# Kernel optimization log

Hardware: AMD Instinct MI355X
Metric: run time of the kernel (lower is better)

## Reference

```python
import jax, jax.numpy as jnp
import numpy as np

HIDDEN = 2048
HEAD_DIM = 128
Q_HEAD = 16
KV_HEAD = 2
MAX_TOKEN = 4096
THETA = 10000
B = 1
S = 2048
SCALER = 1.0 / np.sqrt(HEAD_DIM)


def make_pos_emb():
    # Faithful port of ROPEEmbedding.create_embedding
    i = np.repeat(np.arange(HEAD_DIM // 2), 2)            # [D]
    freq = np.power(float(THETA), -i * 2.0 / HEAD_DIM)    # [D]
    t = np.einsum('i,j->ij', freq, np.arange(MAX_TOKEN, dtype=np.float64))  # [D, T]
    cos = np.cos(t)
    sin = np.sin(t)
    sin[0::2] *= -1.0                                      # negate even rows (even dim indices)
    pe = np.concatenate([cos, sin], axis=0).T              # [T, 2D]
    return jnp.asarray(pe, jnp.float32)


def _flip_pairs(x):
    # swap adjacent pairs along last dim: (x0,x1,x2,x3,..) -> (x1,x0,x3,x2,..)
    b, h, s, d = x.shape
    return x.reshape(b, h, s, d // 2, 2)[..., ::-1].reshape(b, h, s, d)


def _apply_rope(x, pos_emb):
    # x: [B, H, S, D]; pos_emb: [max_token, 2D]
    s = x.shape[2]
    pe = pos_emb[:s]                     # [S, 2D]
    cos = pe[:, :HEAD_DIM]               # [S, D]
    sin = pe[:, HEAD_DIM:]               # [S, D] (signed)
    return x * cos + _flip_pairs(x) * sin


def setup_inputs() -> dict:
    key = jax.random.key(0)
    ks = jax.random.split(key, 5)
    qkv_out = (Q_HEAD + 2 * KV_HEAD) * HEAD_DIM  # 2560
    lim_qkv = 1.0 / np.sqrt(HIDDEN)
    lim_o = 1.0 / np.sqrt(Q_HEAD * HEAD_DIM)
    x = jax.random.normal(ks[0], (B, S, HIDDEN), dtype=jnp.float32)
    w_qkv = jax.random.uniform(ks[1], (qkv_out, HIDDEN), jnp.float32, -lim_qkv, lim_qkv)
    b_qkv = jax.random.uniform(ks[2], (qkv_out,), jnp.float32, -lim_qkv, lim_qkv)
    w_o = jax.random.uniform(ks[3], (HIDDEN, Q_HEAD * HEAD_DIM), jnp.float32, -lim_o, lim_o)
    b_o = jax.random.uniform(ks[4], (HIDDEN,), jnp.float32, -lim_o, lim_o)
    # causal additive mask, as typically passed to this module
    neg = jnp.float32(-1e9)
    attention_mask = jnp.where(
        jnp.tril(jnp.ones((S, S), dtype=bool)), jnp.float32(0.0), neg
    )[None, None, :, :]
    pos_emb = make_pos_emb()
    return {"tensor": x, "attention_mask": attention_mask, "w_qkv": w_qkv,
            "b_qkv": b_qkv, "w_o": w_o, "b_o": b_o, "pos_emb": pos_emb}


def reference(tensor, attention_mask, w_qkv, b_qkv, w_o, b_o, pos_emb):
    b, s, _ = tensor.shape
    qkv = tensor @ w_qkv.T + b_qkv                        # [B, S, 2560]
    dq = HEAD_DIM * Q_HEAD
    dkv = HEAD_DIM * KV_HEAD
    q = qkv[..., :dq].reshape(b, s, Q_HEAD, HEAD_DIM)
    k = qkv[..., dq:dq + dkv].reshape(b, s, KV_HEAD, HEAD_DIM)
    v = qkv[..., dq + dkv:].reshape(b, s, KV_HEAD, HEAD_DIM)
    scale = Q_HEAD // KV_HEAD
    k = jnp.repeat(k, scale, axis=2)                      # [B, S, Q_HEAD, D]
    v = jnp.repeat(v, scale, axis=2)
    q = q.transpose(0, 2, 1, 3)                           # [B, H, S, D]
    k = k.transpose(0, 2, 1, 3)
    v = v.transpose(0, 2, 1, 3)
    q = _apply_rope(q, pos_emb)
    k = _apply_rope(k, pos_emb)
    scores = jnp.einsum('bhqd,bhkd->bhqk', q, k) * SCALER
    scores = scores + attention_mask
    attn = jax.nn.softmax(scores, axis=-1)
    out = jnp.einsum('bhqk,bhkd->bhqd', attn, v)          # [B, H, S, D]
    out = out.transpose(0, 2, 1, 3).reshape(b, s, Q_HEAD * HEAD_DIM)
    return out @ w_o.T + b_o
```

## Files before the change

### kernel.cpp

```cpp
#include <hip/hip_runtime.h>
#include <stdint.h>

#define SQ 2048
#define DH 128
#define SCALER 0.08838834764831845f

typedef float f32x4 __attribute__((ext_vector_type(4)));
typedef short s16x8 __attribute__((ext_vector_type(8)));
typedef short s16x4 __attribute__((ext_vector_type(4)));

__device__ __forceinline__ short f2bf(float f) {
  uint32_t x = __float_as_uint(f);
  uint32_t r = (x + 0x7fffu + ((x >> 16) & 1u)) >> 16;
  return (short)(r & 0xffffu);
}

__device__ __forceinline__ void mfma16(f32x4& d, s16x8 a, s16x8 b) {
  asm("v_mfma_f32_16x16x32_bf16 %0, %1, %2, %0" : "+v"(d) : "v"(a), "v"(b));
}

__device__ __forceinline__ void gload16(const void* g, void* l) {
  __builtin_amdgcn_global_load_lds(
      (__attribute__((address_space(1))) void*)const_cast<void*>(g),
      (__attribute__((address_space(3))) void*)l, 16, 0, 0);
}

__global__ __launch_bounds__(256) void cvt3_bf16(
    const float* __restrict__ a, const float* __restrict__ b,
    const float* __restrict__ c, short* __restrict__ out,
    int na8, int nb8, int nc8) {
  int i = blockIdx.x * 256 + threadIdx.x;
  if (i >= na8 + nb8 + nc8) return;
  const float* src;
  if (i < na8) src = a + (size_t)i * 8;
  else if (i < na8 + nb8) src = b + (size_t)(i - na8) * 8;
  else src = c + (size_t)(i - na8 - nb8) * 8;
  const float4* p = (const float4*)src;
  float4 u = p[0], v = p[1];
  s16x8 o;
  o[0] = f2bf(u.x); o[1] = f2bf(u.y); o[2] = f2bf(u.z); o[3] = f2bf(u.w);
  o[4] = f2bf(v.x); o[5] = f2bf(v.y); o[6] = f2bf(v.z); o[7] = f2bf(v.w);
  *((s16x8*)out + i) = o;
}

template <int MODE>
__global__ __launch_bounds__(256) void gemm_bt_bias(
    const short* __restrict__ A, const short* __restrict__ B,
    const float* __restrict__ bias, float* __restrict__ C,
    const float* __restrict__ pe, short* __restrict__ qws,
    short* __restrict__ kws, short* __restrict__ vtws,
    int M, int N, int K) {
  __shared__ __align__(16) short As_[2][128 * 64];
  __shared__ __align__(16) short Bs_[2][64 * 64];
  const int t = threadIdx.x;
  const int l = t & 63, w = t >> 6;
  const int wr = w >> 1, wc = w & 1;
  const int lr = l & 15, lk = l >> 4;
  const int m0 = blockIdx.y * 128, n0 = blockIdx.x * 64;

  f32x4 acc[4][2] = {};

#define GSTAGE(buf, kt)                                                         \
  {                                                                             \
    const short* ga = A + (size_t)m0 * K + (kt);                                \
    const short* gb = B + (size_t)n0 * K + (kt);                                \
    _Pragma("unroll") for (int i = 0; i < 4; ++i) {                             \
      int j = i * 256 + t;                                                      \
      int lbase = (i * 256 + (t & ~63)) << 4;                                   \
      gload16(ga + (size_t)(j >> 3) * K + ((j & 7) << 3),                       \
              (char*)As_[buf] + lbase);                                         \
    }                                                                           \
    _Pragma("unroll") for (int i = 0; i < 2; ++i) {                             \
      int j = i * 256 + t;                                                      \
      int lbase = (i * 256 + (t & ~63)) << 4;                                   \
      gload16(gb + (size_t)(j >> 3) * K + ((j & 7) << 3),                       \
              (char*)Bs_[buf] + lbase);                                         \
    }                                                                           \
  }

  GSTAGE(0, 0);
  __syncthreads();

  const int nk = K >> 6;
  for (int ki = 0; ki < nk; ++ki) {
    const int cur = ki & 1;
    if (ki + 1 < nk) GSTAGE(cur ^ 1, (ki + 1) << 6);
    const short* As = As_[cur];
    const short* Bs = Bs_[cur];
#pragma unroll
    for (int ks = 0; ks < 2; ++ks) {
      s16x8 af[4], bg[2];
#pragma unroll
      for (int i = 0; i < 4; ++i)
        af[i] = *(const s16x8*)(As + (wr * 64 + i * 16 + lr) * 64 + ks * 32 + lk * 8);
#pragma unroll
      for (int i = 0; i < 2; ++i)
        bg[i] = *(const s16x8*)(Bs + (wc * 32 + i * 16 + lr) * 64 + ks * 32 + lk * 8);
#pragma unroll
      for (int mi = 0; mi < 4; ++mi)
#pragma unroll
        for (int ni = 0; ni < 2; ++ni)
          mfma16(acc[mi][ni], af[mi], bg[ni]);
    }
    __syncthreads();
  }
#undef GSTAGE

  if (MODE == 0) {
#pragma unroll
    for (int mi = 0; mi < 4; ++mi) {
      int row = m0 + wr * 64 + mi * 16 + lk * 4;
#pragma unroll
      for (int ni = 0; ni < 2; ++ni) {
        int col = n0 + wc * 32 + ni * 16 + lr;
        float bv = bias[col];
#pragma unroll
        for (int r = 0; r < 4; ++r)
          C[(size_t)(row + r) * N + col] = acc[mi][ni][r] + bv;
      }
    }
  } else {
    short* Ct = (short*)As_;
    if (n0 < 2304) {
#pragma unroll
      for (int mi = 0; mi < 4; ++mi) {
        int row_l = wr * 64 + mi * 16 + lk * 4;
#pragma unroll
        for (int ni = 0; ni < 2; ++ni) {
          int col_l = wc * 32 + ni * 16 + lr;
          int col = n0 + col_l;
          float bv = bias[col];
          int d = col & 127;
#pragma unroll
          for (int r = 0; r < 4; ++r) {
            float v = acc[mi][ni][r] + bv;
            float p = __shfl_xor(v, 1);
            int s = m0 + row_l + r;
            const float* per = pe + (size_t)s * 256;
            float y = v * per[d] + p * per[128 + d];
            if (n0 < 2048) y *= SCALER;
            Ct[(row_l + r) * 72 + col_l] = f2bf(y);
          }
        }
      }
      __syncthreads();
      if (n0 < 2048) {
        int hq = n0 >> 7, d0 = n0 & 127;
#pragma unroll
        for (int i = 0; i < 4; ++i) {
          int idx = i * 256 + t;
          int sl = idx >> 3, c = idx & 7;
          s16x8 val = *(const s16x8*)(Ct + sl * 72 + c * 8);
          *(s16x8*)(qws + ((size_t)hq * SQ + m0 + sl) * DH + d0 + c * 8) = val;
        }
      } else {
        int hk = (n0 - 2048) >> 7, d0 = (n0 - 2048) & 127;
#pragma unroll
        for (int i = 0; i < 4; ++i) {
          int idx = i * 256 + t;
          int sl = idx >> 3, c = idx & 7;
          s16x8 val = *(const s16x8*)(Ct + sl * 72 + c * 8);
          int slot = ((d0 >> 3) + c) ^ (sl & 15);
          *(s16x8*)(kws + (size_t)hk * SQ * DH + (size_t)(m0 + sl) * DH + slot * 8) = val;
        }
      }
    } else {
      int hk = (n0 - 2304) >> 7, d0 = (n0 - 2304) & 127;
#pragma unroll
      for (int mi = 0; mi < 4; ++mi) {
        int row_l = wr * 64 + mi * 16 + lk * 4;
#pragma unroll
        for (int ni = 0; ni < 2; ++ni) {
          int col_l = wc * 32 + ni * 16 + lr;
          float bv = bias[n0 + col_l];
#pragma unroll
          for (int r = 0; r < 4; ++r)
            Ct[col_l * 136 + row_l + r] = f2bf(acc[mi][ni][r] + bv);
        }
      }
      __syncthreads();
#pragma unroll
      for (int i = 0; i < 4; ++i) {
        int idx = i * 256 + t;
        int dl = idx >> 4, c = idx & 15;
        s16x8 val = *(const s16x8*)(Ct + dl * 136 + c * 8);
        int d = d0 + dl;
        size_t dst = (size_t)hk * DH * SQ + (size_t)d * SQ +
                     (size_t)((m0 >> 6) + (c >> 3)) * 64 +
                     (size_t)(((c & 7) ^ (d & 7)) << 3);
        *(s16x8*)(vtws + dst) = val;
      }
    }
  }
}

__global__ __launch_bounds__(256) void attn_fwd(
    const short* __restrict__ qws, const short* __restrict__ kws,
    const short* __restrict__ vtws, short* __restrict__ attnws) {
  __shared__ __align__(16) short Ks[2][64 * 128];
  __shared__ __align__(16) short Vt[2][128 * 64];
  __shared__ __align__(16) short Ps[4][16 * 72];

  const int bx = blockIdx.x;
  const int h = bx & 15;
  const int i_ = bx >> 4;
  const int qb = (i_ < 16) ? (31 - i_) : (i_ - 16);
  const int hk = h >> 3;
  const int t = threadIdx.x, l = t & 63, w = t >> 6;
  const int lr = l & 15, lk = l >> 4;

  s16x8 qf[4];
  {
    const short* qbase = qws + ((size_t)h * SQ + (size_t)qb * 64 + w * 16) * DH;
#pragma unroll
    for (int kd = 0; kd < 4; ++kd)
      qf[kd] = *(const s16x8*)(qbase + (size_t)lr * DH + kd * 32 + lk * 8);
  }

  f32x4 o[8] = {};
  float m_ = -1e30f, l_ = 0.f;

  const short* gkh = kws + (size_t)hk * SQ * DH;
  const short* gvh = vtws + (size_t)hk * DH * SQ;

#define STAGE(buf, kb)                                                          \
  {                                                                             \
    const short* gk = gkh + (size_t)(kb)*64 * DH;                               \
    const short* gv = gvh + (size_t)(kb)*64;                                    \
    _Pragma("unroll") for (int i = 0; i < 4; ++i) {                             \
      int j = i * 256 + t;                                                      \
      int lbase = (i * 256 + (t & ~63)) << 4;                                   \
      gload16(gk + (size_t)(j >> 4) * DH + ((j & 15) << 3),                     \
              (char*)Ks[buf] + lbase);                                          \
      gload16(gv + (size_t)(j >> 3) * SQ + ((j & 7) << 3),                      \
              (char*)Vt[buf] + lbase);                                          \
    }                                                                           \
  }

  STAGE(0, 0);
  __syncthreads();

  for (int kb = 0; kb <= qb; ++kb) {
    const int cur = kb & 1;
    if (kb < qb) STAGE(cur ^ 1, kb + 1);

    f32x4 sc_[4] = {};
#pragma unroll
    for (int kd = 0; kd < 4; ++kd) {
#pragma unroll
      for (int nt = 0; nt < 4; ++nt) {
        int krow = nt * 16 + lr;
        int slot = (kd * 4 + lk) ^ lr;
        s16x8 kf = *(const s16x8*)(Ks[cur] + krow * 128 + slot * 8);
        mfma16(sc_[nt], kf, qf[kd]);
      }
    }
    if (kb == qb) {
      int qloc = w * 16 + lr;
#pragma unroll
      for (int nt = 0; nt < 4; ++nt)
#pragma unroll
        for (int r = 0; r < 4; ++r) {
          int col = nt * 16 + lk * 4 + r;
          if (col > qloc) sc_[nt][r] = -1e30f;
        }
    }
    {
      float rm = -1e30f;
#pragma unroll
      for (int nt = 0; nt < 4; ++nt)
        rm = fmaxf(rm, fmaxf(fmaxf(sc_[nt][0], sc_[nt][1]),
                             fmaxf(sc_[nt][2], sc_[nt][3])));
      rm = fmaxf(rm, __shfl_xor(rm, 16));
      rm = fmaxf(rm, __shfl_xor(rm, 32));
      float mn = fmaxf(m_, rm);
      float scl = __expf(m_ - mn);
      float rs = 0.f;
#pragma unroll
      for (int nt = 0; nt < 4; ++nt)
#pragma unroll
        for (int r = 0; r < 4; ++r) {
          sc_[nt][r] = __expf(sc_[nt][r] - mn);
          rs += sc_[nt][r];
        }
      rs += __shfl_xor(rs, 16);
      rs += __shfl_xor(rs, 32);
      l_ = l_ * scl + rs;
      m_ = mn;
#pragma unroll
      for (int dt = 0; dt < 8; ++dt)
#pragma unroll
        for (int r = 0; r < 4; ++r) o[dt][r] *= scl;
    }
    {
      short* ps = (short*)Ps[w];
#pragma unroll
      for (int nt = 0; nt < 4; ++nt)
#pragma unroll
        for (int r = 0; r < 4; ++r)
          ps[lr * 72 + nt * 16 + lk * 4 + r] = f2bf(sc_[nt][r]);
    }
    {
      const short* ps = (const short*)Ps[w];
#pragma unroll
      for (int kp = 0; kp < 2; ++kp) {
        s16x8 pbf = *(const s16x8*)(ps + lr * 72 + kp * 32 + lk * 8);
#pragma unroll
        for (int dt = 0; dt < 8; ++dt) {
          int drow = dt * 16 + lr;
          int slot = (kp * 4 + lk) ^ (lr & 7);
          s16x8 vb = *(const s16x8*)(Vt[cur] + drow * 64 + slot * 8);
          mfma16(o[dt], vb, pbf);
        }
      }
    }
    __syncthreads();
  }
#undef STAGE

  {
    int srow = qb * 64 + w * 16 + lr;
#pragma unroll
    for (int dt = 0; dt < 8; ++dt) {
      s16x4 st;
#pragma unroll
      for (int r = 0; r < 4; ++r) st[r] = f2bf(o[dt][r] / l_);
      *(s16x4*)(attnws + (size_t)srow * 2048 + h * DH + dt * 16 + lk * 4) = st;
    }
  }
}

extern "C" void kernel_launch(void* const* d_in, const int* in_sizes, int n_in,
                              void* d_out, int out_size, void* d_ws, size_t ws_size,
                              hipStream_t stream) {
  (void)in_sizes; (void)n_in; (void)out_size; (void)ws_size;
  const float* x     = (const float*)d_in[0];
  const float* w_qkv = (const float*)d_in[2];
  const float* b_qkv = (const float*)d_in[3];
  const float* w_o   = (const float*)d_in[4];
  const float* b_o   = (const float*)d_in[5];
  const float* pe    = (const float*)d_in[6];
  float* out = (float*)d_out;

  short* xb     = (short*)d_ws;
  short* wqkvb  = xb + (size_t)2048 * 2048;
  short* wob    = wqkvb + (size_t)2560 * 2048;
  short* qws    = wob + (size_t)2048 * 2048;
  short* kws    = qws + (size_t)16 * 2048 * 128;
  short* vtws   = kws + (size_t)2 * 2048 * 128;
  short* attnws = vtws + (size_t)2 * 128 * 2048;

  cvt3_bf16<<<6656, 256, 0, stream>>>(x, w_qkv, w_o, xb,
                                      2048 * 2048 / 8, 2560 * 2048 / 8, 2048 * 2048 / 8);
  gemm_bt_bias<1><<<dim3(2560 / 64, 2048 / 128), 256, 0, stream>>>(
      xb, wqkvb, b_qkv, nullptr, pe, qws, kws, vtws, 2048, 2560, 2048);
  attn_fwd<<<512, 256, 0, stream>>>(qws, kws, vtws, attnws);
  gemm_bt_bias<0><<<dim3(2048 / 64, 2048 / 128), 256, 0, stream>>>(
      attnws, wob, b_o, out, nullptr, nullptr, nullptr, nullptr, 2048, 2048, 2048);
}
```

Before: 149.0 us.

## Fuse fp32-to-bf16 conversion into GEMM loads and add lazy softmax rescale

Removes the separate conversion kernel: the GEMMs now read fp32 inputs and weights from global memory into registers, pack them to bf16 with v_cvt_pk_bf16_f32 and write them to LDS after the MFMA step. This drops a full read-convert-write pass over x and both weight matrices, at the cost of register-staged loads replacing the direct global-to-LDS copies and each GEMM block re-converting the same tiles. The attention kernel also skips the running-max rescale of the output accumulators while the new row max stays within 8 of the old one, and raises wave priority around the MFMA loops.

```diff
diff --git a/kernel.cpp b/kernel.cpp
--- a/kernel.cpp
+++ b/kernel.cpp
@@ -15,6 +15,21 @@
   return (short)(r & 0xffffu);
 }
 
+__device__ __forceinline__ uint32_t cvtpk_bf16(float lo, float hi) {
+  uint32_t d;
+  asm("v_cvt_pk_bf16_f32 %0, %1, %2" : "=v"(d) : "v"(lo), "v"(hi));
+  return d;
+}
+
+__device__ __forceinline__ s16x8 pk8(float4 a, float4 b) {
+  union { s16x8 v; uint32_t u[4]; } r;
+  r.u[0] = cvtpk_bf16(a.x, a.y);
+  r.u[1] = cvtpk_bf16(a.z, a.w);
+  r.u[2] = cvtpk_bf16(b.x, b.y);
+  r.u[3] = cvtpk_bf16(b.z, b.w);
+  return r.v;
+}
+
 __device__ __forceinline__ void mfma16(f32x4& d, s16x8 a, s16x8 b) {
   asm("v_mfma_f32_16x16x32_bf16 %0, %1, %2, %0" : "+v"(d) : "v"(a), "v"(b));
 }
@@ -25,27 +40,9 @@
       (__attribute__((address_space(3))) void*)l, 16, 0, 0);
 }
 
-__global__ __launch_bounds__(256) void cvt3_bf16(
-    const float* __restrict__ a, const float* __restrict__ b,
-    const float* __restrict__ c, short* __restrict__ out,
-    int na8, int nb8, int nc8) {
-  int i = blockIdx.x * 256 + threadIdx.x;
-  if (i >= na8 + nb8 + nc8) return;
-  const float* src;
-  if (i < na8) src = a + (size_t)i * 8;
-  else if (i < na8 + nb8) src = b + (size_t)(i - na8) * 8;
-  else src = c + (size_t)(i - na8 - nb8) * 8;
-  const float4* p = (const float4*)src;
-  float4 u = p[0], v = p[1];
-  s16x8 o;
-  o[0] = f2bf(u.x); o[1] = f2bf(u.y); o[2] = f2bf(u.z); o[3] = f2bf(u.w);
-  o[4] = f2bf(v.x); o[5] = f2bf(v.y); o[6] = f2bf(v.z); o[7] = f2bf(v.w);
-  *((s16x8*)out + i) = o;
-}
-
-template <int MODE>
+template <int MODE, int AF32>
 __global__ __launch_bounds__(256) void gemm_bt_bias(
-    const short* __restrict__ A, const short* __restrict__ B,
+    const void* __restrict__ Av, const float* __restrict__ Bf,
     const float* __restrict__ bias, float* __restrict__ C,
     const float* __restrict__ pe, short* __restrict__ qws,
     short* __restrict__ kws, short* __restrict__ vtws,
@@ -59,32 +56,60 @@
   const int m0 = blockIdx.y * 128, n0 = blockIdx.x * 64;
 
   f32x4 acc[4][2] = {};
-
-#define GSTAGE(buf, kt)                                                         \
-  {                                                                             \
-    const short* ga = A + (size_t)m0 * K + (kt);                                \
-    const short* gb = B + (size_t)n0 * K + (kt);                                \
-    _Pragma("unroll") for (int i = 0; i < 4; ++i) {                             \
-      int j = i * 256 + t;                                                      \
-      int lbase = (i * 256 + (t & ~63)) << 4;                                   \
-      gload16(ga + (size_t)(j >> 3) * K + ((j & 7) << 3),                       \
-              (char*)As_[buf] + lbase);                                         \
-    }                                                                           \
-    _Pragma("unroll") for (int i = 0; i < 2; ++i) {                             \
-      int j = i * 256 + t;                                                      \
-      int lbase = (i * 256 + (t & ~63)) << 4;                                   \
-      gload16(gb + (size_t)(j >> 3) * K + ((j & 7) << 3),                       \
-              (char*)Bs_[buf] + lbase);                                         \
-    }                                                                           \
-  }
-
-  GSTAGE(0, 0);
+  float4 ar[8], br[4];
+
+#define GLOAD_A(kt)                                                             \
+  _Pragma("unroll") for (int i = 0; i < 4; ++i) {                               \
+    int c2 = i * 256 + t;                                                       \
+    const float* ga = (const float*)Av + (size_t)(m0 + (c2 >> 3)) * K + (kt) +  \
+                      ((c2 & 7) << 3);                                          \
+    ar[2 * i] = *(const float4*)ga;                                             \
+    ar[2 * i + 1] = *(const float4*)(ga + 4);                                   \
+  }
+#define GWRITE_A(buf)                                                           \
+  _Pragma("unroll") for (int i = 0; i < 4; ++i) {                               \
+    int c2 = i * 256 + t;                                                       \
+    *(s16x8*)(As_[buf] + (c2 >> 3) * 64 + ((c2 & 7) << 3)) =                    \
+        pk8(ar[2 * i], ar[2 * i + 1]);                                          \
+  }
+#define GLOADLDS_A(buf, kt)                                                     \
+  _Pragma("unroll") for (int i = 0; i < 4; ++i) {                               \
+    int j = i * 256 + t;                                                        \
+    int lbase = (i * 256 + (t & ~63)) << 4;                                     \
+    gload16((const short*)Av + (size_t)m0 * K + (kt) + (size_t)(j >> 3) * K +   \
+                ((j & 7) << 3),                                                 \
+            (char*)As_[buf] + lbase);                                           \
+  }
+#define GLOAD_B(kt)                                                             \
+  _Pragma("unroll") for (int i = 0; i < 2; ++i) {                               \
+    int c2 = i * 256 + t;                                                       \
+    const float* gb = Bf + (size_t)(n0 + (c2 >> 3)) * K + (kt) +                \
+                      ((c2 & 7) << 3);                                          \
+    br[2 * i] = *(const float4*)gb;                                             \
+    br[2 * i + 1] = *(const float4*)(gb + 4);                                   \
+  }
+#define GWRITE_B(buf)                                                           \
+  _Pragma("unroll") for (int i = 0; i < 2; ++i) {                               \
+    int c2 = i * 256 + t;                                                       \
+    *(s16x8*)(Bs_[buf] + (c2 >> 3) * 64 + ((c2 & 7) << 3)) =                    \
+        pk8(br[2 * i], br[2 * i + 1]);                                          \
+  }
+
+  if (AF32) { GLOAD_A(0); GWRITE_A(0); }
+  else      { GLOADLDS_A(0, 0); }
+  GLOAD_B(0);
+  GWRITE_B(0);
   __syncthreads();
 
   const int nk = K >> 6;
   for (int ki = 0; ki < nk; ++ki) {
     const int cur = ki & 1;
-    if (ki + 1 < nk) GSTAGE(cur ^ 1, (ki + 1) << 6);
+    const bool pf = (ki + 1 < nk);
+    if (pf) {
+      if (AF32) { GLOAD_A((ki + 1) << 6); }
+      else      { GLOADLDS_A(cur ^ 1, (ki + 1) << 6); }
+      GLOAD_B((ki + 1) << 6);
+    }
     const short* As = As_[cur];
     const short* Bs = Bs_[cur];
 #pragma unroll
@@ -102,9 +127,17 @@
         for (int ni = 0; ni < 2; ++ni)
           mfma16(acc[mi][ni], af[mi], bg[ni]);
     }
+    if (pf) {
+      if (AF32) { GWRITE_A(cur ^ 1); }
+      GWRITE_B(cur ^ 1);
+    }
     __syncthreads();
   }
-#undef GSTAGE
+#undef GLOAD_A
+#undef GWRITE_A
+#undef GLOADLDS_A
+#undef GLOAD_B
+#undef GWRITE_B
 
   if (MODE == 0) {
 #pragma unroll
@@ -245,6 +278,7 @@
     if (kb < qb) STAGE(cur ^ 1, kb + 1);
 
     f32x4 sc_[4] = {};
+    __builtin_amdgcn_s_setprio(1);
 #pragma unroll
     for (int kd = 0; kd < 4; ++kd) {
 #pragma unroll
@@ -255,6 +289,7 @@
         mfma16(sc_[nt], kf, qf[kd]);
       }
     }
+    __builtin_amdgcn_s_setprio(0);
     if (kb == qb) {
       int qloc = w * 16 + lr;
 #pragma unroll
@@ -273,8 +308,8 @@
                              fmaxf(sc_[nt][2], sc_[nt][3])));
       rm = fmaxf(rm, __shfl_xor(rm, 16));
       rm = fmaxf(rm, __shfl_xor(rm, 32));
-      float mn = fmaxf(m_, rm);
-      float scl = __expf(m_ - mn);
+      const bool skip = __all(rm - m_ <= 8.0f);
+      const float mn = skip ? m_ : fmaxf(m_, rm);
       float rs = 0.f;
 #pragma unroll
       for (int nt = 0; nt < 4; ++nt)
@@ -285,12 +320,17 @@
         }
       rs += __shfl_xor(rs, 16);
       rs += __shfl_xor(rs, 32);
-      l_ = l_ * scl + rs;
-      m_ = mn;
-#pragma unroll
-      for (int dt = 0; dt < 8; ++dt)
-#pragma unroll
-        for (int r = 0; r < 4; ++r) o[dt][r] *= scl;
+      if (skip) {
+        l_ += rs;
+      } else {
+        float scl = __expf(m_ - mn);
+        l_ = l_ * scl + rs;
+        m_ = mn;
+#pragma unroll
+        for (int dt = 0; dt < 8; ++dt)
+#pragma unroll
+          for (int r = 0; r < 4; ++r) o[dt][r] *= scl;
+      }
     }
     {
       short* ps = (short*)Ps[w];
@@ -302,6 +342,7 @@
     }
     {
       const short* ps = (const short*)Ps[w];
+      __builtin_amdgcn_s_setprio(1);
 #pragma unroll
       for (int kp = 0; kp < 2; ++kp) {
         s16x8 pbf = *(const s16x8*)(ps + lr * 72 + kp * 32 + lk * 8);
@@ -313,6 +354,7 @@
           mfma16(o[dt], vb, pbf);
         }
       }
+      __builtin_amdgcn_s_setprio(0);
     }
     __syncthreads();
   }
@@ -342,19 +384,14 @@
   const float* pe    = (const float*)d_in[6];
   float* out = (float*)d_out;
 
-  short* xb     = (short*)d_ws;
-  short* wqkvb  = xb + (size_t)2048 * 2048;
-  short* wob    = wqkvb + (size_t)2560 * 2048;
-  short* qws    = wob + (size_t)2048 * 2048;
+  short* qws    = (short*)d_ws;
   short* kws    = qws + (size_t)16 * 2048 * 128;
   short* vtws   = kws + (size_t)2 * 2048 * 128;
   short* attnws = vtws + (size_t)2 * 128 * 2048;
 
-  cvt3_bf16<<<6656, 256, 0, stream>>>(x, w_qkv, w_o, xb,
-                                      2048 * 2048 / 8, 2560 * 2048 / 8, 2048 * 2048 / 8);
-  gemm_bt_bias<1><<<dim3(2560 / 64, 2048 / 128), 256, 0, stream>>>(
-      xb, wqkvb, b_qkv, nullptr, pe, qws, kws, vtws, 2048, 2560, 2048);
+  gemm_bt_bias<1, 1><<<dim3(2560 / 64, 2048 / 128), 256, 0, stream>>>(
+      x, w_qkv, b_qkv, nullptr, pe, qws, kws, vtws, 2048, 2560, 2048);
   attn_fwd<<<512, 256, 0, stream>>>(qws, kws, vtws, attnws);
-  gemm_bt_bias<0><<<dim3(2048 / 64, 2048 / 128), 256, 0, stream>>>(
-      attnws, wob, b_o, out, nullptr, nullptr, nullptr, nullptr, 2048, 2048, 2048);
-}
+  gemm_bt_bias<0, 0><<<dim3(2048 / 64, 2048 / 128), 256, 0, stream>>>(
+      attnws, w_o, b_o, out, nullptr, nullptr, nullptr, nullptr, 2048, 2048, 2048);
+}
```

After: 155.5 us. 1.04x slower.
